# Kernel tuning notes

Hardware: AMD Instinct MI355X
Metric: run time of the kernel (lower is better)

## Reference

```python
import jax, jax.numpy as jnp
import numpy as np

NUM_HEADS = 16
HEAD_DIM = 64  # d_out // num_heads


def setup_inputs() -> dict:
    key = jax.random.key(0)
    ks = jax.random.split(key, 6)
    d_in, d_out, b, t = 1024, 1024, 2, 2048
    s = 0.02
    return {
        "x": jax.random.normal(ks[0], (b, t, d_in), jnp.float32),
        "Wq": jax.random.normal(ks[1], (d_in, d_out), jnp.float32) * s,
        "Wk": jax.random.normal(ks[2], (d_in, d_out), jnp.float32) * s,
        "Wv": jax.random.normal(ks[3], (d_in, d_out), jnp.float32) * s,
        "Wo": jax.random.normal(ks[4], (d_out, d_out), jnp.float32) * s,
        "bo": jnp.zeros((d_out,), jnp.float32),
    }


def reference(x, Wq, Wk, Wv, Wo, bo):
    b, t, _ = x.shape
    H, hd = NUM_HEADS, HEAD_DIM
    # qkv projections (no bias), split into heads: [b, H, t, hd]
    q = (x @ Wq).reshape(b, t, H, hd).transpose(0, 2, 1, 3)
    k = (x @ Wk).reshape(b, t, H, hd).transpose(0, 2, 1, 3)
    v = (x @ Wv).reshape(b, t, H, hd).transpose(0, 2, 1, 3)
    # raw scores, causal mask (masked_fill with -1e9 BEFORE the 1/sqrt(hd) scale,
    # matching the source exactly), then scaled softmax
    scores = jnp.einsum("bhqd,bhkd->bhqk", q, k)
    causal = jnp.triu(jnp.ones((t, t), dtype=bool), k=1)
    scores = jnp.where(causal[None, None], jnp.float32(-1e9), scores)
    attn = jax.nn.softmax(scores / jnp.sqrt(jnp.float32(hd)), axis=-1)
    # dropout is identity in eval mode
    ctx = jnp.einsum("bhqk,bhkd->bhqd", attn, v)  # [b, H, t, hd]
    ctx = ctx.transpose(0, 2, 1, 3).reshape(b, t, H * hd)
    return ctx @ Wo + bo
```

## Files before the change

### kernel.cpp

```cpp
#include <hip/hip_runtime.h>


#define SEQ   2048
#define DMODEL 1024
#define NH    16
#define HD    64
#define MROWS 4096

typedef __attribute__((ext_vector_type(4))) float f32x4;
typedef __attribute__((ext_vector_type(16))) float f32x16;
typedef __attribute__((ext_vector_type(8))) short short8;
typedef __attribute__((ext_vector_type(4))) unsigned int u32x4;

#define MFMA16(a, b, c) __builtin_amdgcn_mfma_f32_16x16x32_bf16((a), (b), (c), 0, 0, 0)
#define MFMA32(a, b, c) __builtin_amdgcn_mfma_f32_32x32x16_bf16((a), (b), (c), 0, 0, 0)

__device__ __forceinline__ unsigned short f2bf(float f) {
  union { float f; unsigned u; } v; v.f = f;
  return (unsigned short)((v.u + 0x7fffu + ((v.u >> 16) & 1u)) >> 16);
}

__device__ __forceinline__ float exp2x(float x) {
#if __has_builtin(__builtin_amdgcn_exp2f)
  return __builtin_amdgcn_exp2f(x);
#else
  float r; asm("v_exp_f32 %0, %1" : "=v"(r) : "v"(x)); return r;
#endif
}

__device__ __forceinline__ unsigned cvt_pk(float lo, float hi) {
  unsigned r;
  asm volatile("v_cvt_pk_bf16_f32 %0, %1, %2" : "=v"(r) : "v"(lo), "v"(hi));
  return r;
}

__device__ __forceinline__ void pls(unsigned& a, unsigned& b) {
  asm("v_permlane32_swap_b32 %0, %1" : "+v"(a), "+v"(b));
}

__device__ __forceinline__ short8 as_short8(u32x4 v) {
  union { u32x4 u; short8 s; } x; x.u = v; return x.s;
}

__device__ __forceinline__ f32x4 zero4() {
  f32x4 z; z[0] = 0.f; z[1] = 0.f; z[2] = 0.f; z[3] = 0.f; return z;
}

__device__ __forceinline__ void async16(const void* g, void* l) {
  __builtin_amdgcn_global_load_lds(
      (const __attribute__((address_space(1))) unsigned int*)g,
      (__attribute__((address_space(3))) unsigned int*)l, 16, 0, 0);
}

__global__ __launch_bounds__(256) void prep(
    const float* __restrict__ x, const float* __restrict__ Wq,
    const float* __restrict__ Wk, const float* __restrict__ Wv,
    const float* __restrict__ Wo, unsigned short* __restrict__ xb,
    unsigned short* __restrict__ Wt, unsigned short* __restrict__ WoT) {
  __shared__ unsigned short tile[64][65];
  const int bx = blockIdx.x;
  if (bx < 2048) {
    int i = bx * 256 + threadIdx.x;
    const float4* p = (const float4*)x;
    float4 a = p[2 * i];
    float4 b = p[2 * i + 1];
    short8 o;
    o[0] = (short)f2bf(a.x); o[1] = (short)f2bf(a.y);
    o[2] = (short)f2bf(a.z); o[3] = (short)f2bf(a.w);
    o[4] = (short)f2bf(b.x); o[5] = (short)f2bf(b.y);
    o[6] = (short)f2bf(b.z); o[7] = (short)f2bf(b.w);
    *(short8*)&xb[(size_t)i * 8] = o;
    return;
  }
  const int id2 = bx - 2048;
  const int m = id2 >> 8;
  const float* W = (m == 0) ? Wq : (m == 1) ? Wk : (m == 2) ? Wv : Wo;
  unsigned short* D = (m == 3) ? WoT : Wt + (size_t)m * 1024 * 1024;
  const int tid = id2 & 255;
  const int kb = (tid >> 4) * 64, nb = (tid & 15) * 64;
  const int t = threadIdx.x;
  const int tx = t & 63, ty = t >> 6;
#pragma unroll
  for (int rr = 0; rr < 16; rr++) {
    int r = ty * 16 + rr;
    tile[r][tx] = f2bf(W[(size_t)(kb + r) * 1024 + nb + tx]);
  }
  __syncthreads();
#pragma unroll
  for (int rr = 0; rr < 16; rr++) {
    int r = ty * 16 + rr;
    D[(size_t)(nb + r) * 1024 + kb + tx] = tile[tx][r];
  }
}

template <int MODE, int WMF>
__global__ __launch_bounds__(256) void gemm_bt(
    const unsigned short* __restrict__ A, const unsigned short* __restrict__ Bt,
    unsigned short* __restrict__ Qo, unsigned short* __restrict__ Ko,
    unsigned short* __restrict__ Vo, float* __restrict__ out,
    const float* __restrict__ bo) {
  constexpr int K = 1024;
  constexpr int BM = WMF * 32;
  constexpr int NW = K / 64;
  constexpr int ASZ = BM * 32;
  constexpr int BSZ = 128 * 32;
  __shared__ __align__(16) unsigned short smem[4 * ASZ + 4 * BSZ];
  unsigned short* Asb = smem;
  unsigned short* Bsb = smem + 4 * ASZ;
  const int t = threadIdx.x;
  const int lane = t & 63;
  const int w = t >> 6;
  const int lr = lane & 15, kf = lane >> 4;
  const int wr = w >> 1, wc = w & 1;

  const int nwg = gridDim.x * gridDim.y;
  const int id = blockIdx.y * gridDim.x + blockIdx.x;
  const int swz = (id & 7) * (nwg >> 3) + (id >> 3);
  const int bx = swz % gridDim.x, by = swz / gridDim.x;

  const int rowbase = bx * BM;
  const int colbase = by * 128;

  const unsigned short* Ab = A + (size_t)rowbase * K;
  const unsigned short* Bb = Bt + (size_t)colbase * K;

  f32x4 acc[WMF][4];
#pragma unroll
  for (int m = 0; m < WMF; m++)
#pragma unroll
    for (int n = 0; n < 4; n++) acc[m][n] = zero4();

  auto stage = [&](int buf, int wi) {
#pragma unroll
    for (int sub = 0; sub < 2; sub++) {
      int k0 = (2 * wi + sub) * 32;
      unsigned short* Ad = Asb + ((size_t)buf * 2 + sub) * ASZ;
      unsigned short* Bd = Bsb + ((size_t)buf * 2 + sub) * BSZ;
#pragma unroll
      for (int i = 0; i < BM / 64; i++) {
        int f = i * 256 + t;
        int c = f ^ ((f >> 3) & 3);
        int row = c >> 2;
        int col = (c & 3) << 3;
        async16(Ab + (size_t)row * K + k0 + col, (char*)Ad + (size_t)f * 16);
      }
#pragma unroll
      for (int i = 0; i < 2; i++) {
        int f = i * 256 + t;
        int c = f ^ ((f >> 3) & 3);
        int row = c >> 2;
        int col = (c & 3) << 3;
        async16(Bb + (size_t)row * K + k0 + col, (char*)Bd + (size_t)f * 16);
      }
    }
  };

  auto compute = [&](int buf, int sub) {
    const unsigned short* As = Asb + ((size_t)buf * 2 + sub) * ASZ;
    const unsigned short* Bs = Bsb + ((size_t)buf * 2 + sub) * BSZ;
    short8 av[WMF], bv[4];
#pragma unroll
    for (int m = 0; m < WMF; m++) {
      int row = wr * (WMF * 16) + m * 16 + lr;
      int idx = (row * 32 + kf * 8) ^ (((row >> 1) & 3) << 3);
      av[m] = *(const short8*)&As[idx];
    }
#pragma unroll
    for (int n = 0; n < 4; n++) {
      int row = wc * 64 + n * 16 + lr;
      int idx = (row * 32 + kf * 8) ^ (((row >> 1) & 3) << 3);
      bv[n] = *(const short8*)&Bs[idx];
    }
    __builtin_amdgcn_s_setprio(1);
#pragma unroll
    for (int m = 0; m < WMF; m++)
#pragma unroll
      for (int n = 0; n < 4; n++) acc[m][n] = MFMA16(av[m], bv[n], acc[m][n]);
    __builtin_amdgcn_s_setprio(0);
  };

  stage(0, 0);
  int cur = 0;

  for (int wi = 0; wi < NW; wi++) {
    if (wi + 1 < NW) {
      stage(cur ^ 1, wi + 1);
      if constexpr (MODE == 0) asm volatile("s_waitcnt vmcnt(8)" ::: "memory");
      else                     asm volatile("s_waitcnt vmcnt(6)" ::: "memory");
    } else {
      asm volatile("s_waitcnt vmcnt(0)" ::: "memory");
    }
    __builtin_amdgcn_s_barrier();

    compute(cur, 0);
    compute(cur, 1);

    __builtin_amdgcn_s_barrier();
    cur ^= 1;
  }

  if constexpr (MODE == 0) {
    if (colbase < 2048) {
      const int selq = colbase >> 10;
      unsigned short* dst = selq ? Ko : Qo;
      const float sc = selq ? 1.0f : 0.18033688011112042f;
#pragma unroll
      for (int n = 0; n < 4; n++) {
        int c = colbase + wc * 64 + n * 16 + lr;
        int hh = (c >> 6) & 15;
        int dd = c & 63;
#pragma unroll
        for (int m = 0; m < WMF; m++) {
          int r0 = rowbase + wr * (WMF * 16) + m * 16 + kf * 4;
#pragma unroll
          for (int i = 0; i < 4; i++) {
            int r = r0 + i;
            int bi = r >> 11;
            int tq = r & 2047;
            dst[((size_t)(bi * NH + hh) * SEQ + tq) * HD + dd] = f2bf(acc[m][n][i] * sc);
          }
        }
      }
    } else {
      unsigned short* tr = smem;
#pragma unroll
      for (int n = 0; n < 4; n++) {
        int ccol = wc * 64 + n * 16 + lr;
#pragma unroll
        for (int m = 0; m < WMF; m++) {
#pragma unroll
          for (int i = 0; i < 4; i++) {
            int rrow = wr * (WMF * 16) + m * 16 + kf * 4 + i;
            tr[ccol * 136 + rrow] = f2bf(acc[m][n][i]);
          }
        }
      }
      __syncthreads();
      const int bi2 = rowbase >> 11;
      const int tq0 = rowbase & 2047;
#pragma unroll
      for (int k2 = 0; k2 < 8; k2++) {
        int u = k2 * 256 + t;
        int cc = u >> 4, seg = u & 15;
        int c = colbase + cc;
        int hh = (c >> 6) & 15, dd = c & 63;
        short8 v8 = *(const short8*)&tr[cc * 136 + seg * 8];
        *(short8*)&Vo[((size_t)(bi2 * NH + hh) * HD + dd) * SEQ + tq0 + seg * 8] = v8;
      }
    }
  } else {
#pragma unroll
    for (int n = 0; n < 4; n++) {
      int c = colbase + wc * 64 + n * 16 + lr;
      float bias = bo[c];
#pragma unroll
      for (int m = 0; m < WMF; m++) {
        int r0 = rowbase + wr * (WMF * 16) + m * 16 + kf * 4;
#pragma unroll
        for (int i = 0; i < 4; i++) {
          out[(size_t)(r0 + i) * 1024 + c] = acc[m][n][i] + bias;
        }
      }
    }
  }
}

__global__ __launch_bounds__(256) void attn_fwd(
    const unsigned short* __restrict__ Q, const unsigned short* __restrict__ K,
    const unsigned short* __restrict__ Vt, unsigned short* __restrict__ ctx) {
  const int bh = blockIdx.x;
  const int y = blockIdx.y;
  const int qt = (y < 8) ? (15 - y) : (y - 8);
  const int bi = bh >> 4, hh = bh & 15;
  const int t = threadIdx.x, lane = t & 63, w = t >> 6;
  const int qc = lane & 31, hi = lane >> 5;

  __shared__ __align__(16) unsigned short Ks[2][2][64 * 64];
  __shared__ __align__(16) unsigned short Vs[2][2][64 * 64];

  const unsigned short* Qb = Q + (size_t)bh * SEQ * HD;
  const unsigned short* Kb = K + (size_t)bh * SEQ * HD;
  const unsigned short* Vb = Vt + (size_t)bh * HD * SEQ;

  const int qrow = qt * 128 + w * 32;
  short8 qv[4];
#pragma unroll
  for (int c = 0; c < 4; c++)
    qv[c] = *(const short8*)&Qb[(size_t)(qrow + qc) * HD + c * 16 + hi * 8];

  f32x16 o0, o1;
#pragma unroll
  for (int i = 0; i < 16; i++) { o0[i] = 0.f; o1[i] = 0.f; }
  float l_acc = 0.f;

  const int ktmax = 2 * qt + (w >> 1);
  const int NP = qt + 1;

  auto stage = [&](int buf, int p) {
#pragma unroll
    for (int sub = 0; sub < 2; sub++) {
      int kt = 2 * p + sub;
#pragma unroll
      for (int i2 = 0; i2 < 2; i2++) {
        int f = i2 * 256 + t;
        int c = f ^ ((f >> 3) & 7);
        async16(Kb + (size_t)kt * 64 * HD + (size_t)c * 8,
                (char*)&Ks[buf][sub][0] + (size_t)f * 16);
        int d = c >> 3, ko = (c & 7) << 3;
        async16(Vb + (size_t)d * SEQ + (size_t)kt * 64 + ko,
                (char*)&Vs[buf][sub][0] + (size_t)f * 16);
      }
    }
  };

  auto tile = [&](const unsigned short* Kt, const unsigned short* Vtile, int kt) {
    f32x16 s0, s1;
#pragma unroll
    for (int i = 0; i < 16; i++) { s0[i] = 0.f; s1[i] = 0.f; }
    __builtin_amdgcn_s_setprio(1);
#pragma unroll
    for (int c = 0; c < 4; c++) {
      int i0 = (qc * 64 + c * 16 + hi * 8) ^ ((qc & 7) << 3);
      s0 = MFMA32(*(const short8*)&Kt[i0], qv[c], s0);
      int r1 = 32 + qc;
      int i1 = (r1 * 64 + c * 16 + hi * 8) ^ ((r1 & 7) << 3);
      s1 = MFMA32(*(const short8*)&Kt[i1], qv[c], s1);
    }
    __builtin_amdgcn_s_setprio(0);

    if (kt == ktmax) {
      const int qg = qrow + qc;
#pragma unroll
      for (int reg = 0; reg < 16; reg++) {
        int rloc = (reg & 3) + 8 * (reg >> 2) + 4 * hi;
        int kg = kt * 64 + rloc;
        if (kg > qg) s0[reg] = -1e30f;
        if (kg + 32 > qg) s1[reg] = -1e30f;
      }
    }

    unsigned w0[8], w1[8];
    float psA = 0.f, psB = 0.f;
#pragma unroll
    for (int j = 0; j < 8; j++) {
      float a0 = exp2x(s0[2 * j]), b0 = exp2x(s0[2 * j + 1]);
      float a1 = exp2x(s1[2 * j]), b1 = exp2x(s1[2 * j + 1]);
      psA += a0 + b0;
      psB += a1 + b1;
      w0[j] = cvt_pk(a0, b0);
      w1[j] = cvt_pk(a1, b1);
    }
    l_acc += psA + psB;

    __builtin_amdgcn_s_setprio(1);
#pragma unroll
    for (int h2 = 0; h2 < 2; h2++) {
      unsigned* pw = h2 ? w1 : w0;
#pragma unroll
      for (int cc = 0; cc < 2; cc++) {
        unsigned a0 = pw[cc * 4 + 0], b0 = pw[cc * 4 + 2];
        unsigned a1 = pw[cc * 4 + 1], b1 = pw[cc * 4 + 3];
        pls(a0, b0);
        pls(a1, b1);
        u32x4 pf; pf[0] = a0; pf[1] = a1; pf[2] = b0; pf[3] = b1;
        short8 pfrag = as_short8(pf);
        int c2 = h2 * 2 + cc;
        int ia = (qc * 64 + c2 * 16 + hi * 8) ^ ((qc & 7) << 3);
        o0 = MFMA32(*(const short8*)&Vtile[ia], pfrag, o0);
        int rb = 32 + qc;
        int ib = (rb * 64 + c2 * 16 + hi * 8) ^ ((rb & 7) << 3);
        o1 = MFMA32(*(const short8*)&Vtile[ib], pfrag, o1);
      }
    }
    __builtin_amdgcn_s_setprio(0);
  };

  stage(0, 0);
  int cur = 0;

  for (int p = 0; p < NP; p++) {
    if (p + 1 < NP) {
      stage(cur ^ 1, p + 1);
      asm volatile("s_waitcnt vmcnt(8)" ::: "memory");
    } else {
      asm volatile("s_waitcnt vmcnt(0)" ::: "memory");
    }
    __builtin_amdgcn_s_barrier();

    if (2 * p <= ktmax)     tile(&Ks[cur][0][0], &Vs[cur][0][0], 2 * p);
    if (2 * p + 1 <= ktmax) tile(&Ks[cur][1][0], &Vs[cur][1][0], 2 * p + 1);

    __builtin_amdgcn_s_barrier();
    cur ^= 1;
  }

  float l = l_acc + __shfl_xor(l_acc, 32);
  float inv = 1.0f / l;
  const size_t rowoff = ((size_t)bi * SEQ + qrow + qc) * DMODEL + hh * HD;
#pragma unroll
  for (int g = 0; g < 4; g++) {
    unsigned pa = cvt_pk(o0[4 * g] * inv, o0[4 * g + 1] * inv);
    unsigned pb = cvt_pk(o0[4 * g + 2] * inv, o0[4 * g + 3] * inv);
    uint2 vv; vv.x = pa; vv.y = pb;
    *(uint2*)&ctx[rowoff + 8 * g + 4 * hi] = vv;
    unsigned pc = cvt_pk(o1[4 * g] * inv, o1[4 * g + 1] * inv);
    unsigned pd = cvt_pk(o1[4 * g + 2] * inv, o1[4 * g + 3] * inv);
    uint2 ww; ww.x = pc; ww.y = pd;
    *(uint2*)&ctx[rowoff + 32 + 8 * g + 4 * hi] = ww;
  }
}

extern "C" void kernel_launch(void* const* d_in, const int* in_sizes, int n_in,
                              void* d_out, int out_size, void* d_ws, size_t ws_size,
                              hipStream_t stream) {
  const float* x  = (const float*)d_in[0];
  const float* Wq = (const float*)d_in[1];
  const float* Wk = (const float*)d_in[2];
  const float* Wv = (const float*)d_in[3];
  const float* Wo = (const float*)d_in[4];
  const float* bo = (const float*)d_in[5];
  float* out = (float*)d_out;

  unsigned short* xb   = (unsigned short*)d_ws;
  unsigned short* Wt   = xb + (size_t)MROWS * DMODEL;
  unsigned short* WoT  = Wt + (size_t)3 * 1024 * 1024;
  unsigned short* Qb   = WoT + (size_t)1024 * 1024;
  unsigned short* Kb   = Qb + (size_t)MROWS * DMODEL;
  unsigned short* Vb   = Kb + (size_t)MROWS * DMODEL;
  unsigned short* ctxb = Vb + (size_t)MROWS * DMODEL;

  prep<<<3072, 256, 0, stream>>>(x, Wq, Wk, Wv, Wo, xb, Wt, WoT);

  gemm_bt<0, 4><<<dim3(32, 24), 256, 0, stream>>>(xb, Wt, Qb, Kb, Vb, nullptr, nullptr);
  attn_fwd<<<dim3(32, 16), 256, 0, stream>>>(Qb, Kb, Vb, ctxb);
  gemm_bt<1, 2><<<dim3(64, 8), 256, 0, stream>>>(ctxb, WoT, nullptr, nullptr, nullptr, out, bo);
}
```

Measured before the change: 104.8 us.

## Split long causal query tiles across two blocks with a combine kernel

The eight longest query tiles of causal attention are each split along the key dimension into two halves processed by separate blocks. Each half writes unnormalized bf16 partial outputs and row sums into reused workspace. A new combine kernel adds the halves and normalizes them. This is meant to balance per-block work and raise the grid from 512 to 768 blocks, at the cost of an extra launch, extra memory traffic and bf16 rounding of the partials. Combining partials by plain addition is only correct because the softmax uses no running max.

Result: slower. 112.6 us (+7.5%).

```diff
diff --git a/kernel.cpp b/kernel.cpp
--- a/kernel.cpp
+++ b/kernel.cpp
@@ -18,6 +18,10 @@
 __device__ __forceinline__ unsigned short f2bf(float f) {
   union { float f; unsigned u; } v; v.f = f;
   return (unsigned short)((v.u + 0x7fffu + ((v.u >> 16) & 1u)) >> 16);
+}
+
+__device__ __forceinline__ float bf2f(unsigned short s) {
+  union { unsigned u; float f; } v; v.u = ((unsigned)s) << 16; return v.f;
 }
 
 __device__ __forceinline__ float exp2x(float x) {
@@ -267,10 +271,28 @@
 
 __global__ __launch_bounds__(256) void attn_fwd(
     const unsigned short* __restrict__ Q, const unsigned short* __restrict__ K,
-    const unsigned short* __restrict__ Vt, unsigned short* __restrict__ ctx) {
+    const unsigned short* __restrict__ Vt, unsigned short* __restrict__ ctx,
+    unsigned short* __restrict__ pO, float* __restrict__ pl) {
   const int bh = blockIdx.x;
   const int y = blockIdx.y;
-  const int qt = (y < 8) ? (15 - y) : (y - 8);
+  int qt, p_begin, p_end, pidx;
+  bool partial;
+  if (y < 16) {
+    qt = 15 - (y >> 1);
+    const int half = y & 1;
+    const int NP = qt + 1;
+    const int h0 = (NP + 1) >> 1;
+    p_begin = half ? h0 : 0;
+    p_end = half ? NP : h0;
+    partial = true;
+    pidx = (bh * 8 + (qt - 8)) * 2 + half;
+  } else {
+    qt = 23 - y;
+    p_begin = 0;
+    p_end = qt + 1;
+    partial = false;
+    pidx = 0;
+  }
   const int bi = bh >> 4, hh = bh & 15;
   const int t = threadIdx.x, lane = t & 63, w = t >> 6;
   const int qc = lane & 31, hi = lane >> 5;
@@ -294,7 +316,6 @@
   float l_acc = 0.f;
 
   const int ktmax = 2 * qt + (w >> 1);
-  const int NP = qt + 1;
 
   auto stage = [&](int buf, int p) {
 #pragma unroll
@@ -375,11 +396,11 @@
     __builtin_amdgcn_s_setprio(0);
   };
 
-  stage(0, 0);
+  stage(0, p_begin);
   int cur = 0;
 
-  for (int p = 0; p < NP; p++) {
-    if (p + 1 < NP) {
+  for (int p = p_begin; p < p_end; p++) {
+    if (p + 1 < p_end) {
       stage(cur ^ 1, p + 1);
       asm volatile("s_waitcnt vmcnt(8)" ::: "memory");
     } else {
@@ -394,19 +415,63 @@
     cur ^= 1;
   }
 
-  float l = l_acc + __shfl_xor(l_acc, 32);
-  float inv = 1.0f / l;
-  const size_t rowoff = ((size_t)bi * SEQ + qrow + qc) * DMODEL + hh * HD;
-#pragma unroll
-  for (int g = 0; g < 4; g++) {
-    unsigned pa = cvt_pk(o0[4 * g] * inv, o0[4 * g + 1] * inv);
-    unsigned pb = cvt_pk(o0[4 * g + 2] * inv, o0[4 * g + 3] * inv);
-    uint2 vv; vv.x = pa; vv.y = pb;
-    *(uint2*)&ctx[rowoff + 8 * g + 4 * hi] = vv;
-    unsigned pc = cvt_pk(o1[4 * g] * inv, o1[4 * g + 1] * inv);
-    unsigned pd = cvt_pk(o1[4 * g + 2] * inv, o1[4 * g + 3] * inv);
-    uint2 ww; ww.x = pc; ww.y = pd;
-    *(uint2*)&ctx[rowoff + 32 + 8 * g + 4 * hi] = ww;
+  if (partial) {
+    const size_t rowoff = ((size_t)pidx * 128 + w * 32 + qc) * 64;
+#pragma unroll
+    for (int g = 0; g < 4; g++) {
+      unsigned pa = cvt_pk(o0[4 * g], o0[4 * g + 1]);
+      unsigned pb = cvt_pk(o0[4 * g + 2], o0[4 * g + 3]);
+      uint2 vv; vv.x = pa; vv.y = pb;
+      *(uint2*)&pO[rowoff + 8 * g + 4 * hi] = vv;
+      unsigned pc = cvt_pk(o1[4 * g], o1[4 * g + 1]);
+      unsigned pd = cvt_pk(o1[4 * g + 2], o1[4 * g + 3]);
+      uint2 ww; ww.x = pc; ww.y = pd;
+      *(uint2*)&pO[rowoff + 32 + 8 * g + 4 * hi] = ww;
+    }
+    float l = l_acc + __shfl_xor(l_acc, 32);
+    if (hi == 0) pl[pidx * 128 + w * 32 + qc] = l;
+  } else {
+    float l = l_acc + __shfl_xor(l_acc, 32);
+    float inv = 1.0f / l;
+    const size_t rowoff = ((size_t)bi * SEQ + qrow + qc) * DMODEL + hh * HD;
+#pragma unroll
+    for (int g = 0; g < 4; g++) {
+      unsigned pa = cvt_pk(o0[4 * g] * inv, o0[4 * g + 1] * inv);
+      unsigned pb = cvt_pk(o0[4 * g + 2] * inv, o0[4 * g + 3] * inv);
+      uint2 vv; vv.x = pa; vv.y = pb;
+      *(uint2*)&ctx[rowoff + 8 * g + 4 * hi] = vv;
+      unsigned pc = cvt_pk(o1[4 * g] * inv, o1[4 * g + 1] * inv);
+      unsigned pd = cvt_pk(o1[4 * g + 2] * inv, o1[4 * g + 3] * inv);
+      uint2 ww; ww.x = pc; ww.y = pd;
+      *(uint2*)&ctx[rowoff + 32 + 8 * g + 4 * hi] = ww;
+    }
+  }
+}
+
+__global__ __launch_bounds__(256) void combine(
+    const unsigned short* __restrict__ pO, const float* __restrict__ pl,
+    unsigned short* __restrict__ ctx) {
+  const int bh = blockIdx.x, q8 = blockIdx.y;
+  const int bi = bh >> 4, hh = bh & 15;
+  const int t = threadIdx.x;
+  const int r = t >> 1, dh = (t & 1) << 5;
+  const int pbase = (bh * 8 + q8) * 2;
+  const size_t a0 = ((size_t)pbase * 128 + r) * 64 + dh;
+  const size_t a1 = ((size_t)(pbase + 1) * 128 + r) * 64 + dh;
+  const float l = pl[pbase * 128 + r] + pl[(pbase + 1) * 128 + r];
+  const float inv = 1.0f / l;
+  const size_t co = ((size_t)bi * SEQ + (8 + q8) * 128 + r) * DMODEL + hh * HD + dh;
+#pragma unroll
+  for (int c = 0; c < 4; c++) {
+    short8 va = *(const short8*)&pO[a0 + c * 8];
+    short8 vb = *(const short8*)&pO[a1 + c * 8];
+    short8 o;
+#pragma unroll
+    for (int j = 0; j < 8; j++) {
+      float f = (bf2f((unsigned short)va[j]) + bf2f((unsigned short)vb[j])) * inv;
+      o[j] = (short)f2bf(f);
+    }
+    *(short8*)&ctx[co + c * 8] = o;
   }
 }
 
@@ -429,9 +494,13 @@
   unsigned short* Vb   = Kb + (size_t)MROWS * DMODEL;
   unsigned short* ctxb = Vb + (size_t)MROWS * DMODEL;
 
+  unsigned short* pO = xb;
+  float* pl = (float*)Wt;
+
   prep<<<3072, 256, 0, stream>>>(x, Wq, Wk, Wv, Wo, xb, Wt, WoT);
 
   gemm_bt<0, 4><<<dim3(32, 24), 256, 0, stream>>>(xb, Wt, Qb, Kb, Vb, nullptr, nullptr);
-  attn_fwd<<<dim3(32, 16), 256, 0, stream>>>(Qb, Kb, Vb, ctxb);
+  attn_fwd<<<dim3(32, 24), 256, 0, stream>>>(Qb, Kb, Vb, ctxb, pO, pl);
+  combine<<<dim3(32, 8), 256, 0, stream>>>(pO, pl, ctxb);
   gemm_bt<1, 2><<<dim3(64, 8), 256, 0, stream>>>(ctxb, WoT, nullptr, nullptr, nullptr, out, bo);
 }
```
